# Kernel tuning notes

Measured on AMD Instinct MI355X. Metric: run time of the kernel, lower is better.

The kernel has to match this reference:

```python
import jax, jax.numpy as jnp
import numpy as np
from jax import lax

B, T, D = 4, 2048, 1024
H, DK, DV = 8, 128, 256
K_CONV = 4
EPS_RMS = 1e-5


def _causal_conv_silu(x, w, b):
    # x: (B,T,C), w: (C,1,K) depthwise, b: (C,)
    C = x.shape[-1]
    xc = jnp.transpose(x, (0, 2, 1))  # (B,C,T)
    y = lax.conv_general_dilated(
        xc, w, window_strides=(1,), padding=[(K_CONV - 1, 0)],
        dimension_numbers=('NCH', 'OIH', 'NCH'), feature_group_count=C)
    y = y + b[None, :, None]
    y = jnp.transpose(y, (0, 2, 1))  # (B,T,C)
    return jax.nn.silu(y)


def _l2norm(x, eps=1e-12):
    n = jnp.sqrt(jnp.sum(x * x, axis=-1, keepdims=True))
    return x / jnp.maximum(n, eps)


def setup_inputs() -> dict:
    key = jax.random.key(0)
    ks = jax.random.split(key, 20)
    s = 0.02
    inp = {
        'hidden_states': jax.random.normal(ks[0], (B, T, D), jnp.float32),
        'previous_state': jax.random.normal(ks[1], (B, H, DK, DV), jnp.float32) * 0.1,
        'Wq': jax.random.normal(ks[2], (D, H * DK), jnp.float32) * s,
        'Wk': jax.random.normal(ks[3], (D, H * DK), jnp.float32) * s,
        'Wv': jax.random.normal(ks[4], (D, H * DV), jnp.float32) * s,
        'Wa': jax.random.normal(ks[5], (D, H), jnp.float32) * s,
        'Wb': jax.random.normal(ks[6], (D, H), jnp.float32) * s,
        'Wg': jax.random.normal(ks[7], (D, H * DV), jnp.float32) * s,
        'Wo': jax.random.normal(ks[8], (H * DV, D), jnp.float32) * s,
        'qc_w': jax.random.normal(ks[9], (H * DK, 1, K_CONV), jnp.float32) * 0.25,
        'qc_b': jnp.zeros((H * DK,), jnp.float32),
        'kc_w': jax.random.normal(ks[10], (H * DK, 1, K_CONV), jnp.float32) * 0.25,
        'kc_b': jnp.zeros((H * DK,), jnp.float32),
        'vc_w': jax.random.normal(ks[11], (H * DV, 1, K_CONV), jnp.float32) * 0.25,
        'vc_b': jnp.zeros((H * DV,), jnp.float32),
        'o_norm_w': jnp.ones((DV,), jnp.float32),
    }
    A = jax.random.uniform(ks[12], (H,), jnp.float32, 1e-4, 16.0)
    inp['A_log'] = jnp.log(A)
    # depth_init=True: dt in [1e-4, 1e-3]
    u = jax.random.uniform(ks[13], (H,), jnp.float32)
    dt = jnp.exp(u * (np.log(1e-3) - np.log(1e-4)) + np.log(1e-4))
    inp['dt_bias'] = dt + jnp.log(-jnp.expm1(-dt))
    return inp


def reference(hidden_states, previous_state, Wq, Wk, Wv, Wa, Wb, Wg, Wo,
              qc_w, qc_b, kc_w, kc_b, vc_w, vc_b, o_norm_w, A_log, dt_bias):
    b, t, _ = hidden_states.shape
    # projections + causal depthwise conv + silu
    q = _causal_conv_silu(hidden_states @ Wq, qc_w, qc_b).reshape(b, t, H, DK)
    k = _causal_conv_silu(hidden_states @ Wk, kc_w, kc_b).reshape(b, t, H, DK)
    v = _causal_conv_silu(hidden_states @ Wv, vc_w, vc_b).reshape(b, t, H, DV)
    # gates
    g = -jnp.exp(A_log) * jax.nn.softplus(hidden_states @ Wa + dt_bias)  # (B,T,H)
    alpha = jnp.exp(g)
    beta = jax.nn.sigmoid(hidden_states @ Wb)  # (B,T,H)
    # qk L2 norm
    q = _l2norm(q)
    k = _l2norm(k)

    def step(state, xs):
        q_t, k_t, v_t, a_t, b_t = xs
        o_t = jnp.einsum('bhkv,bhk->bhv', state, q_t)  # read state BEFORE update
        delta = v_t - jnp.einsum('bhkv,bhk->bhv', state, k_t)
        state = a_t[..., None, None] * state + \
            b_t[..., None, None] * jnp.einsum('bhv,bhk->bhkv', delta, k_t)
        return state, o_t

    xs = (jnp.transpose(q, (1, 0, 2, 3)), jnp.transpose(k, (1, 0, 2, 3)),
          jnp.transpose(v, (1, 0, 2, 3)), jnp.transpose(alpha, (1, 0, 2)),
          jnp.transpose(beta, (1, 0, 2)))
    final_state, o = lax.scan(step, previous_state, xs)
    o = jnp.transpose(o, (1, 0, 2, 3))  # (B,T,H,DV)
    # gated RMSNorm per head-v dim
    gate = (hidden_states @ Wg).reshape(b, t, H, DV)
    of = o.astype(jnp.float32)
    var = jnp.mean(of * of, axis=-1, keepdims=True)
    o = (o_norm_w * (of * lax.rsqrt(var + EPS_RMS)).astype(o.dtype)) * jax.nn.sigmoid(gate)
    out = o.reshape(b, t, H * DV) @ Wo  # (B,T,D)
    return out, final_state
```

## Files before the change

kernel.cpp:

```cpp
#include <hip/hip_runtime.h>
#include <stdint.h>

typedef unsigned short u16;
typedef unsigned int u32;

#define DEVFN __device__ __forceinline__

constexpr int CB = 4;
constexpr int CT = 2048;
constexpr int CD = 1024;
constexpr int CH = 8;
constexpr int CDK = 128;
constexpr int CDV = 256;
constexpr long NROW = (long)CB * CT;

DEVFN float b2f(u16 s){ return __uint_as_float(((u32)s) << 16); }
DEVFN u16 f2b(float f){
  u32 u = __float_as_uint(f);
  u32 r = (u + 0x7fffu + ((u >> 16) & 1u)) >> 16;
  return (u16)r;
}
DEVFN float sigm(float x){ return 1.f / (1.f + expf(-x)); }
DEVFN int swz3(int r){ return (r ^ (r >> 2)) & 3; }

__global__ void cast_f32_bf16_k(const float* __restrict__ in, u16* __restrict__ out, long n4){
  long i = (long)blockIdx.x * blockDim.x + threadIdx.x;
  long stride = (long)gridDim.x * blockDim.x;
  for (; i < n4; i += stride){
    float4 v = ((const float4*)in)[i];
    ushort4 r;
    r.x = f2b(v.x); r.y = f2b(v.y); r.z = f2b(v.z); r.w = f2b(v.w);
    ((ushort4*)out)[i] = r;
  }
}

__global__ __launch_bounds__(256) void transpose_all_k(
    const float* __restrict__ Wq, const float* __restrict__ Wk, const float* __restrict__ Wv,
    const float* __restrict__ Wg, const float* __restrict__ Wo,
    u16* __restrict__ Wqkvt, u16* __restrict__ Wgt, u16* __restrict__ Wot)
{
  int bid = blockIdx.x;
  const float* W; u16* Wt; int K, N, local;
  if (bid < 1024){ W = Wq; Wt = Wqkvt; K = 1024; N = 1024; local = bid; }
  else if (bid < 2048){ W = Wk; Wt = Wqkvt + (size_t)1024 * 1024; K = 1024; N = 1024; local = bid - 1024; }
  else if (bid < 4096){ W = Wv; Wt = Wqkvt + (size_t)2048 * 1024; K = 1024; N = 2048; local = bid - 2048; }
  else if (bid < 6144){ W = Wg; Wt = Wgt; K = 1024; N = 2048; local = bid - 4096; }
  else { W = Wo; Wt = Wot; K = 2048; N = 1024; local = bid - 6144; }
  int sh = (N == 1024) ? 5 : 6;
  int bx = local & ((1 << sh) - 1), by = local >> sh;
  int n0 = bx * 32, k0 = by * 32;

  __shared__ float tile[32][33];
  int tx = threadIdx.x & 31, ty = threadIdx.x >> 5;
  #pragma unroll
  for (int i = 0; i < 4; i++)
    tile[ty + 8*i][tx] = W[(long)(k0 + ty + 8*i) * N + n0 + tx];
  __syncthreads();
  #pragma unroll
  for (int i = 0; i < 4; i++){
    int nn = ty + 8*i;
    Wt[(long)(n0 + nn) * K + k0 + tx] = f2b(tile[tx][nn]);
  }
}

typedef __bf16 bf16x8 __attribute__((ext_vector_type(8)));
typedef float f32x4 __attribute__((ext_vector_type(4)));

DEVFN void store_c(float* p, float v){ *p = v; }
DEVFN void store_c(u16* p, float v){ *p = f2b(v); }

DEVFN void gload16(const void* g, void* l){
  __builtin_amdgcn_global_load_lds((__attribute__((address_space(1))) void*)g,
                                   (__attribute__((address_space(3))) void*)l, 16, 0, 0);
}

template <typename OutT>
__global__ __launch_bounds__(256) void gemm128_k(
    const u16* __restrict__ A, const u16* __restrict__ Bt, OutT* __restrict__ C,
    int M, int N, int K)
{
  __shared__ u16 As[2][128 * 64];
  __shared__ u16 Bs[2][128 * 64];
  int tid = threadIdx.x;
  int lane = tid & 63, wv = tid >> 6;
  int wm = wv & 1, wn = wv >> 1;
  int l15 = lane & 15, lhi = lane >> 4;
  int m0 = blockIdx.y * 128, n0 = blockIdx.x * 128;
  const u16* Ab = A + (long)m0 * K;
  const u16* Bb = Bt + (long)n0 * K;

  auto stage = [&](int t, int bf){
    int k0 = t * 64;
    #pragma unroll
    for (int p = 0; p < 4; p++){
      int X = p * 256 + tid;
      int r = X >> 3, jj = X & 7;
      gload16(Ab + (long)r * K + k0 + ((jj ^ (r & 7)) * 8), &As[bf][(size_t)X * 8]);
    }
    #pragma unroll
    for (int p = 0; p < 4; p++){
      int X = p * 256 + tid;
      int r = X >> 3, jj = X & 7;
      gload16(Bb + (long)r * K + k0 + ((jj ^ (r & 7)) * 8), &Bs[bf][(size_t)X * 8]);
    }
  };

  f32x4 acc[4][4] = {};

  stage(0, 0);
  int T = K >> 6;
  for (int t = 0; t < T; t++){
    int bf = t & 1;
    if (t + 1 < T){
      stage(t + 1, bf ^ 1);
      asm volatile("s_waitcnt vmcnt(8)" ::: "memory");
    } else {
      asm volatile("s_waitcnt vmcnt(0)" ::: "memory");
    }
    __builtin_amdgcn_s_barrier();

    #pragma unroll
    for (int kk = 0; kk < 64; kk += 32){
      int s = (kk >> 3) + lhi;
      bf16x8 av[4], bv[4];
      #pragma unroll
      for (int m = 0; m < 4; m++){
        int r = wm * 64 + m * 16 + l15;
        av[m] = *(const bf16x8*)&As[bf][r * 64 + ((s ^ (r & 7)) * 8)];
      }
      #pragma unroll
      for (int n = 0; n < 4; n++){
        int r = wn * 64 + n * 16 + l15;
        bv[n] = *(const bf16x8*)&Bs[bf][r * 64 + ((s ^ (r & 7)) * 8)];
      }
      #pragma unroll
      for (int m = 0; m < 4; m++)
        #pragma unroll
        for (int n = 0; n < 4; n++)
          acc[m][n] = __builtin_amdgcn_mfma_f32_16x16x32_bf16(av[m], bv[n], acc[m][n], 0, 0, 0);
    }
    asm volatile("" ::: "memory");
    __builtin_amdgcn_s_barrier();
  }

  #pragma unroll
  for (int m = 0; m < 4; m++)
    #pragma unroll
    for (int n = 0; n < 4; n++)
      #pragma unroll
      for (int j = 0; j < 4; j++){
        long row = m0 + wm * 64 + m * 16 + lhi * 4 + j;
        long col = n0 + wn * 64 + n * 16 + l15;
        store_c(&C[row * (long)N + col], acc[m][n][j]);
      }
}

__global__ __launch_bounds__(256) void build_wab_k(
    const float* __restrict__ Wa, const float* __restrict__ Wb, u16* __restrict__ Wab)
{
  int idx = blockIdx.x * 256 + threadIdx.x;
  int c = idx >> 10, k = idx & 1023;
  float v = (c < 8) ? Wa[k * 8 + c] : Wb[k * 8 + (c - 8)];
  Wab[c * 1024 + k] = f2b(v);
}

__global__ __launch_bounds__(256) void ab_mfma_k(
    const u16* __restrict__ Xb, const u16* __restrict__ Wab,
    const float* __restrict__ A_log, const float* __restrict__ dt_bias,
    float* __restrict__ alpha, float* __restrict__ beta)
{
  __shared__ u16 Ws[16 * 1024];
  int tid = threadIdx.x, lane = tid & 63, wv = tid >> 6;
  #pragma unroll
  for (int p = 0; p < 8; p++){
    int X = p * 256 + tid;
    int r = X >> 7, s = X & 127;
    gload16(Wab + r * 1024 + (s ^ (r & 7)) * 8, &Ws[(size_t)X * 8]);
  }
  int l15 = lane & 15, lhi = lane >> 4;
  int row0 = blockIdx.x * 64 + wv * 16;
  const u16* Arow = Xb + (long)(row0 + l15) * 1024 + lhi * 8;
  __syncthreads();

  f32x4 acc = {0.f, 0.f, 0.f, 0.f};
  #pragma unroll 8
  for (int ks = 0; ks < 32; ks++){
    bf16x8 av = *(const bf16x8*)(Arow + ks * 32);
    int slot = ks * 4 + lhi;
    bf16x8 bv = *(const bf16x8*)&Ws[l15 * 1024 + (slot ^ (l15 & 7)) * 8];
    acc = __builtin_amdgcn_mfma_f32_16x16x32_bf16(av, bv, acc, 0, 0, 0);
  }

  int col = l15;
  float nA = 0.f, db = 0.f;
  if (col < 8){ nA = -expf(A_log[col]); db = dt_bias[col]; }
  #pragma unroll
  for (int j = 0; j < 4; j++){
    long row = row0 + lhi * 4 + j;
    float v = acc[j];
    if (col < 8){
      float xv = v + db;
      float sp = fmaxf(xv, 0.f) + log1pf(expf(-fabsf(xv)));
      alpha[row * 8 + col] = expf(nA * sp);
    } else {
      beta[row * 8 + (col - 8)] = sigm(v);
    }
  }
}

template<int DH, bool NORM>
__global__ __launch_bounds__(DH/2) void conv_silu8_k(
    const u16* __restrict__ pre, int cstride, const float* __restrict__ cw,
    const float* __restrict__ cb, u16* __restrict__ out)
{
  int idx = blockIdx.x;
  int h = idx & 7;
  int tg = (idx >> 3) & 255;
  int b = idx >> 11;
  int t0 = tg * 8;
  int tidx = threadIdx.x;
  int c2 = tidx * 2;
  int ch = h * DH + c2;
  const u16* base = pre + ((long)b * CT) * cstride + ch;
  float w0a = cw[ch * 4 + 0], w0b = cw[ch * 4 + 1], w0c = cw[ch * 4 + 2], w0d = cw[ch * 4 + 3];
  float w1a = cw[(ch + 1) * 4 + 0], w1b = cw[(ch + 1) * 4 + 1], w1c = cw[(ch + 1) * 4 + 2], w1d = cw[(ch + 1) * 4 + 3];
  float bs0 = cb[ch], bs1 = cb[ch + 1];

  u32 rr[11];
  #pragma unroll
  for (int i = 0; i < 11; i++){
    int t = t0 - 3 + i;
    rr[i] = (t >= 0) ? *(const u32*)(base + (long)t * cstride) : 0u;
  }
  #pragma unroll
  for (int tt = 0; tt < 8; tt++){
    int t = t0 + tt;
    float x0a = b2f((u16)(rr[tt] & 0xffffu)),     x1a = b2f((u16)(rr[tt] >> 16));
    float x0b = b2f((u16)(rr[tt + 1] & 0xffffu)), x1b = b2f((u16)(rr[tt + 1] >> 16));
    float x0c = b2f((u16)(rr[tt + 2] & 0xffffu)), x1c = b2f((u16)(rr[tt + 2] >> 16));
    float x0d = b2f((u16)(rr[tt + 3] & 0xffffu)), x1d = b2f((u16)(rr[tt + 3] >> 16));
    float a0 = fmaf(w0a, x0a, fmaf(w0b, x0b, fmaf(w0c, x0c, fmaf(w0d, x0d, bs0))));
    float a1 = fmaf(w1a, x1a, fmaf(w1b, x1b, fmaf(w1c, x1c, fmaf(w1d, x1d, bs1))));
    float y0 = a0 * sigm(a0), y1 = a1 * sigm(a1);
    if (NORM){
      float ss = y0 * y0 + y1 * y1;
      #pragma unroll
      for (int off = 1; off < 64; off <<= 1) ss += __shfl_xor(ss, off);
      float inv = 1.f / fmaxf(sqrtf(ss), 1e-12f);
      y0 *= inv; y1 *= inv;
    }
    u32 r = (u32)f2b(y0) | ((u32)f2b(y1) << 16);
    *(u32*)(out + (((long)b * CT + t) * 8 + h) * DH + c2) = r;
  }
}

__global__ __launch_bounds__(256) void chunk_meta_k(
    const u16* __restrict__ qn, const u16* __restrict__ kn, const u16* __restrict__ vn,
    const float* __restrict__ alpha, const float* __restrict__ beta,
    u16* __restrict__ TGK_g, u16* __restrict__ TVT_g, u16* __restrict__ P_g,
    u16* __restrict__ KTS_g, float* __restrict__ scal_g)
{
  int bid = blockIdx.x;
  int c = bid & 63, bh = bid >> 6;
  int b = bh >> 3, h = bh & 7;
  long rowb = (long)b * CT + c * 32;
  int tid = threadIdx.x, lane = tid & 63, wv = tid >> 6;
  int l15 = lane & 15, lhi = lane >> 4;
  int mt = wv & 1, nt = wv >> 1;

  __shared__ u16 Kc[4096], Qc[4096], Vl[8192];
  __shared__ u16 Vt[10240];
  __shared__ u16 KTG[5120];
  __shared__ u16 TinvL[1280];
  __shared__ float Al[32 * 33];
  __shared__ float al_s[32], be_s[32], cums[33], bscal[32], gsl[32];

  #pragma unroll
  for (int p = 0; p < 2; p++){
    int X = p * 256 + tid; int r = X >> 4, jj = X & 15;
    gload16(kn + ((rowb + r) * 8 + h) * 128 + (jj ^ (r & 7)) * 8, &Kc[(size_t)X * 8]);
  }
  #pragma unroll
  for (int p = 0; p < 2; p++){
    int X = p * 256 + tid; int r = X >> 4, jj = X & 15;
    gload16(qn + ((rowb + r) * 8 + h) * 128 + (jj ^ (r & 7)) * 8, &Qc[(size_t)X * 8]);
  }
  #pragma unroll
  for (int p = 0; p < 4; p++){
    int X = p * 256 + tid; int r = X >> 5, cc = X & 31;
    gload16(vn + ((rowb + r) * 8 + h) * 256 + cc * 8, &Vl[(size_t)X * 8]);
  }
  if (tid < 32) al_s[tid] = alpha[(rowb + tid) * 8 + h];
  else if (tid < 64) be_s[tid - 32] = beta[(rowb + tid - 32) * 8 + h];
  __syncthreads();
  if (tid == 0){
    float cacc = 0.f; cums[0] = 0.f;
    for (int j = 0; j < 32; j++){ cacc += logf(al_s[j]); cums[j + 1] = cacc; }
  }
  __syncthreads();
  if (tid < 32){
    bscal[tid] = be_s[tid] * expf(cums[32] - cums[tid + 1]);
    gsl[tid] = expf(cums[tid]);
  }
  asm volatile("s_waitcnt vmcnt(0)" ::: "memory");
  __syncthreads();

  #pragma unroll
  for (int i = 0; i < 16; i++){
    u32 lo = Vl[(2 * i) * 256 + tid];
    u32 hi = Vl[(2 * i + 1) * 256 + tid];
    *(u32*)&Vt[tid * 40 + 2 * i] = lo | (hi << 16);
  }

  f32x4 rk = {0.f,0.f,0.f,0.f}, rq = {0.f,0.f,0.f,0.f};
  int ra = mt * 16 + l15, rb = nt * 16 + l15;
  #pragma unroll
  for (int ks = 0; ks < 4; ks++){
    int slot = ks * 4 + lhi;
    bf16x8 ak = *(const bf16x8*)&Kc[ra * 128 + (slot ^ (ra & 7)) * 8];
    bf16x8 aq = *(const bf16x8*)&Qc[ra * 128 + (slot ^ (ra & 7)) * 8];
    bf16x8 bk = *(const bf16x8*)&Kc[rb * 128 + (slot ^ (rb & 7)) * 8];
    rk = __builtin_amdgcn_mfma_f32_16x16x32_bf16(ak, bk, rk, 0, 0, 0);
    rq = __builtin_amdgcn_mfma_f32_16x16x32_bf16(aq, bk, rq, 0, 0, 0);
  }
  int s_ = nt * 16 + l15;
  long pb_ = (long)bid * 1024;
  #pragma unroll
  for (int j = 0; j < 4; j++){
    int i_ = mt * 16 + lhi * 4 + j;
    float e = (s_ < i_) ? expf(cums[i_] - cums[s_ + 1]) * be_s[s_] : 0.f;
    Al[i_ * 33 + s_] = rk[j] * e;
    P_g[pb_ + i_ * 32 + s_] = f2b(rq[j] * e);
  }
  __syncthreads();

  if (tid < 32){
    float x[32];
    #pragma unroll
    for (int i = 0; i < 32; i++) x[i] = (i == tid) ? 1.f : 0.f;
    #pragma unroll
    for (int s = 0; s < 31; s++){
      float xs = x[s];
      #pragma unroll
      for (int i = s + 1; i < 32; i++) x[i] = fmaf(-Al[i * 33 + s], xs, x[i]);
    }
    #pragma unroll
    for (int i = 0; i < 32; i++) TinvL[i * 40 + tid] = f2b(x[i]);
    scal_g[(long)bid * 48 + tid] = gsl[tid];
    if (tid == 0) scal_g[(long)bid * 48 + 32] = expf(cums[32]);
  } else if (tid >= 64){
    int t0 = tid - 64;
    #pragma unroll
    for (int e2 = 0; e2 < 22; e2++){
      int e = t0 + e2 * 192;
      if (e < 4096){
        int k = e >> 5, s2 = e & 31;
        int slot = k >> 3;
        float kv = b2f(Kc[s2 * 128 + (slot ^ (s2 & 7)) * 8 + (k & 7)]);
        KTS_g[(long)bid * 4096 + k * 32 + s2] = f2b(kv * bscal[s2]);
        KTG[k * 40 + s2] = f2b(kv * gsl[s2]);
      }
    }
  }
  __syncthreads();

  long tb = (long)bid * 4096;
  #pragma unroll
  for (int p = 0; p < 4; p++){
    int idx = wv * 4 + p; int ts = idx >> 3, tk = idx & 7;
    bf16x8 aT = *(const bf16x8*)&TinvL[(ts * 16 + l15) * 40 + lhi * 8];
    bf16x8 bK2 = *(const bf16x8*)&KTG[(tk * 16 + l15) * 40 + lhi * 8];
    f32x4 z = {0.f,0.f,0.f,0.f};
    f32x4 d = __builtin_amdgcn_mfma_f32_16x16x32_bf16(aT, bK2, z, 0, 0, 0);
    #pragma unroll
    for (int j = 0; j < 4; j++)
      TGK_g[tb + (ts * 16 + lhi * 4 + j) * 128 + tk * 16 + l15] = f2b(d[j]);
  }
  long vb = (long)bid * 8192;
  #pragma unroll
  for (int p = 0; p < 8; p++){
    int idx = wv * 8 + p; int tv = idx >> 1, ts2 = idx & 1;
    bf16x8 aV = *(const bf16x8*)&Vt[(tv * 16 + l15) * 40 + lhi * 8];
    bf16x8 bT2 = *(const bf16x8*)&TinvL[(ts2 * 16 + l15) * 40 + lhi * 8];
    f32x4 z = {0.f,0.f,0.f,0.f};
    f32x4 d = __builtin_amdgcn_mfma_f32_16x16x32_bf16(aV, bT2, z, 0, 0, 0);
    #pragma unroll
    for (int j = 0; j < 4; j++)
      TVT_g[vb + (tv * 16 + lhi * 4 + j) * 32 + ts2 * 16 + l15] = f2b(d[j]);
  }
}

__global__ __launch_bounds__(256) void chunk_scan_k(
    const u16* __restrict__ qn, const u16* __restrict__ TGK_g, const u16* __restrict__ TVT_g,
    const u16* __restrict__ P_g, const u16* __restrict__ KTS_g,
    const float* __restrict__ scal_g, const float* __restrict__ prev,
    u16* __restrict__ obuf, float* __restrict__ fstate)
{
  int bid = blockIdx.x;
  int bh = bid & 31, vs = bid >> 5;
  int b = bh >> 3, h = bh & 7;
  int tid = threadIdx.x, lane = tid & 63, wv = tid >> 6;
  int l15 = lane & 15, lhi = lane >> 4;
  int mv = wv & 1, nn = wv >> 1;

  __shared__ u16 TG[2][4096];
  __shared__ u16 Qc[2][4096];
  __shared__ u16 TVs[2][1024];
  __shared__ float scal[2][48];
  __shared__ u16 KT[2][4096];
  __shared__ u16 Ps[2][1024];
  __shared__ u16 Sb[32 * 136];
  __shared__ u16 Ub[32 * 40];

  auto issue_g1 = [&](int c, int bf){
    long cb_ = (long)bh * 64 + c;
    const u16* Tb_ = TGK_g + cb_ * 4096;
    #pragma unroll
    for (int p = 0; p < 2; p++){
      int X = p * 256 + tid; int r = X >> 4, jj = X & 15;
      gload16(Tb_ + r * 128 + (jj ^ (r & 7)) * 8, &TG[bf][(size_t)X * 8]);
    }
    long rowb = (long)b * CT + c * 32;
    #pragma unroll
    for (int p = 0; p < 2; p++){
      int X = p * 256 + tid; int r = X >> 4, jj = X & 15;
      gload16(qn + ((rowb + r) * 8 + h) * 128 + (jj ^ (r & 7)) * 8, &Qc[bf][(size_t)X * 8]);
    }
    if (lane < 32){
      int X = wv * 32 + lane; int r = X >> 2, jj = X & 3;
      gload16(TVT_g + cb_ * 8192 + (vs * 32 + r) * 32 + (jj ^ swz3(r)) * 8, &TVs[bf][(size_t)X * 8]);
    }
    long sbase = cb_ * 48;
    #pragma unroll
    for (int p = 0; p < 3; p++){
      int X = wv * 3 + p;
      if (lane == 0) gload16(scal_g + sbase + X * 4, &scal[bf][X * 4]);
    }
  };
  auto issue_g2 = [&](int c, int bf){
    long cb_ = (long)bh * 64 + c;
    const u16* Kb_ = KTS_g + cb_ * 4096;
    #pragma unroll
    for (int p = 0; p < 2; p++){
      int X = p * 256 + tid; int r = X >> 2, jj = X & 3;
      gload16(Kb_ + (r * 4 + (jj ^ swz3(r))) * 8, &KT[bf][(size_t)X * 8]);
    }
    if (lane < 32){
      int X = wv * 32 + lane; int r = X >> 2, jj = X & 3;
      gload16(P_g + cb_ * 1024 + (r * 4 + (jj ^ swz3(r))) * 8, &Ps[bf][(size_t)X * 8]);
    }
  };

  issue_g1(0, 0);
  issue_g2(0, 0);
  f32x4 st[4];
  {
    const float* pbv = prev + ((long)bh * 128) * 256 + vs * 32;
    #pragma unroll
    for (int tt = 0; tt < 4; tt++){
      int k = (nn * 4 + tt) * 16 + l15;
      #pragma unroll
      for (int j = 0; j < 4; j++){
        int v = mv * 16 + lhi * 4 + j;
        st[tt][j] = pbv[(long)k * 256 + v];
      }
    }
  }
  #pragma unroll
  for (int tt = 0; tt < 4; tt++){
    int k = (nn * 4 + tt) * 16 + l15;
    #pragma unroll
    for (int j = 0; j < 4; j++){
      int v = mv * 16 + lhi * 4 + j;
      Sb[v * 136 + k] = f2b(st[tt][j]);
    }
  }
  asm volatile("s_waitcnt vmcnt(3) lgkmcnt(0)" ::: "memory");
  __builtin_amdgcn_s_barrier();

  int rv = mv * 16 + l15, ri = nn * 16 + l15;
  for (int c = 0; c < 64; ++c){
    int bf = c & 1;
    f32x4 us = {0.f,0.f,0.f,0.f}, o1 = {0.f,0.f,0.f,0.f};
    #pragma unroll
    for (int ks = 0; ks < 4; ks++){
      bf16x8 aS = *(const bf16x8*)&Sb[rv * 136 + ks * 32 + lhi * 8];
      int slot = ks * 4 + lhi;
      bf16x8 bT = *(const bf16x8*)&TG[bf][ri * 128 + (slot ^ (ri & 7)) * 8];
      bf16x8 bQ = *(const bf16x8*)&Qc[bf][ri * 128 + (slot ^ (ri & 7)) * 8];
      us = __builtin_amdgcn_mfma_f32_16x16x32_bf16(aS, bT, us, 0, 0, 0);
      o1 = __builtin_amdgcn_mfma_f32_16x16x32_bf16(aS, bQ, o1, 0, 0, 0);
    }
    if (c + 1 < 64) issue_g1(c + 1, bf ^ 1);
    #pragma unroll
    for (int j = 0; j < 4; j++){
      int v = mv * 16 + lhi * 4 + j;
      float tv = b2f(TVs[bf][v * 32 + ((ri >> 3) ^ swz3(v)) * 8 + (ri & 7)]);
      Ub[v * 40 + ri] = f2b(tv - us[j]);
    }
    asm volatile("s_waitcnt lgkmcnt(0)" ::: "memory");
    if (c + 1 < 64) asm volatile("s_waitcnt vmcnt(8)" ::: "memory");
    else            asm volatile("s_waitcnt vmcnt(0)" ::: "memory");
    __builtin_amdgcn_s_barrier();

    float Gt = scal[bf][32];
    f32x4 oacc;
    {
      bf16x8 aU = *(const bf16x8*)&Ub[rv * 40 + lhi * 8];
      bf16x8 bP = *(const bf16x8*)&Ps[bf][ri * 32 + (lhi ^ swz3(ri)) * 8];
      f32x4 z = {0.f,0.f,0.f,0.f};
      oacc = __builtin_amdgcn_mfma_f32_16x16x32_bf16(aU, bP, z, 0, 0, 0);
      #pragma unroll
      for (int tt = 0; tt < 4; tt++){
        int rk_ = (nn * 4 + tt) * 16 + l15;
        bf16x8 bK = *(const bf16x8*)&KT[bf][rk_ * 32 + (lhi ^ swz3(rk_)) * 8];
        f32x4 ci = st[tt] * Gt;
        st[tt] = __builtin_amdgcn_mfma_f32_16x16x32_bf16(aU, bK, ci, 0, 0, 0);
      }
    }
    {
      float gi = scal[bf][ri];
      ushort4 pk;
      pk.x = f2b(oacc[0] + gi * o1[0]);
      pk.y = f2b(oacc[1] + gi * o1[1]);
      pk.z = f2b(oacc[2] + gi * o1[2]);
      pk.w = f2b(oacc[3] + gi * o1[3]);
      *(ushort4*)&obuf[(((long)bh * CT) + c * 32 + ri) * 256 + vs * 32 + mv * 16 + lhi * 4] = pk;
    }
    if (c + 1 < 64) issue_g2(c + 1, bf ^ 1);
    #pragma unroll
    for (int tt = 0; tt < 4; tt++){
      int k = (nn * 4 + tt) * 16 + l15;
      #pragma unroll
      for (int j = 0; j < 4; j++){
        int v = mv * 16 + lhi * 4 + j;
        Sb[v * 136 + k] = f2b(st[tt][j]);
      }
    }
    asm volatile("s_waitcnt lgkmcnt(0)" ::: "memory");
    if (c + 1 < 64) asm volatile("s_waitcnt vmcnt(3)" ::: "memory");
    else            asm volatile("s_waitcnt vmcnt(0)" ::: "memory");
    __builtin_amdgcn_s_barrier();
  }

  {
    float* fb = fstate + ((long)bh * 128) * 256 + vs * 32;
    #pragma unroll
    for (int tt = 0; tt < 4; tt++){
      int k = (nn * 4 + tt) * 16 + l15;
      #pragma unroll
      for (int j = 0; j < 4; j++){
        int v = mv * 16 + lhi * 4 + j;
        fb[(long)k * 256 + v] = st[tt][j];
      }
    }
  }
}

__global__ __launch_bounds__(256) void rms_gate_k(
    const u16* __restrict__ o, const u16* __restrict__ gate,
    const float* __restrict__ nw, u16* __restrict__ ofin)
{
  long idx = (long)blockIdx.x * 4 + (threadIdx.x >> 6);
  int lane = threadIdx.x & 63;
  int h = (int)(idx & 7);
  long bt = idx >> 3;
  int b = (int)(bt >> 11);
  long t = bt & (CT - 1);
  long obase = (((long)(b * 8 + h)) * CT + t) * CDV + lane * 4;
  long base = idx * CDV + lane * 4;
  ushort4 o4 = *(const ushort4*)(o + obase);
  float ox = b2f(o4.x), oy = b2f(o4.y), oz = b2f(o4.z), ow = b2f(o4.w);
  float ss = ox*ox + oy*oy + oz*oz + ow*ow;
  #pragma unroll
  for (int off = 1; off < 64; off <<= 1) ss += __shfl_xor(ss, off);
  float r = rsqrtf(ss * (1.f / CDV) + 1e-5f);
  ushort4 g4 = *(const ushort4*)(gate + base);
  float w0 = nw[lane*4], w1 = nw[lane*4+1], w2 = nw[lane*4+2], w3 = nw[lane*4+3];
  ushort4 res;
  res.x = f2b(ox * r * w0 * sigm(b2f(g4.x)));
  res.y = f2b(oy * r * w1 * sigm(b2f(g4.y)));
  res.z = f2b(oz * r * w2 * sigm(b2f(g4.z)));
  res.w = f2b(ow * r * w3 * sigm(b2f(g4.w)));
  *(ushort4*)(ofin + base) = res;
}

extern "C" void kernel_launch(void* const* d_in, const int* in_sizes, int n_in,
                              void* d_out, int out_size, void* d_ws, size_t ws_size,
                              hipStream_t stream)
{
  (void)in_sizes; (void)n_in; (void)out_size; (void)ws_size;
  const float* X    = (const float*)d_in[0];
  const float* prev = (const float*)d_in[1];
  const float* Wq   = (const float*)d_in[2];
  const float* Wk   = (const float*)d_in[3];
  const float* Wv   = (const float*)d_in[4];
  const float* Wa   = (const float*)d_in[5];
  const float* Wb   = (const float*)d_in[6];
  const float* Wg   = (const float*)d_in[7];
  const float* Wo   = (const float*)d_in[8];
  const float* qcw  = (const float*)d_in[9];
  const float* qcb  = (const float*)d_in[10];
  const float* kcw  = (const float*)d_in[11];
  const float* kcb  = (const float*)d_in[12];
  const float* vcw  = (const float*)d_in[13];
  const float* vcb  = (const float*)d_in[14];
  const float* onw  = (const float*)d_in[15];
  const float* Alog = (const float*)d_in[16];
  const float* dtb  = (const float*)d_in[17];

  float* out = (float*)d_out;
  float* fstate = out + (long)CB * CT * CD;

  char* ws = (char*)d_ws;
  size_t off = 0;
  auto alloc = [&](size_t bytes) -> char* {
    char* p = ws + off;
    off += (bytes + 255) & ~(size_t)255;
    return p;
  };
  u16* Xb     = (u16*)alloc(NROW * CD * 2);
  u16* Wqkvt  = (u16*)alloc((size_t)4096 * 1024 * 2);
  u16* Wgt    = (u16*)alloc((size_t)2048 * 1024 * 2);
  u16* Wot    = (u16*)alloc((size_t)1024 * 2048 * 2);
  u16* qkvpre = (u16*)alloc(NROW * 4096 * 2);
  u16* gpre   = (u16*)alloc(NROW * 2048 * 2);
  float* alpha = (float*)alloc(NROW * 8 * 4);
  float* beta  = (float*)alloc(NROW * 8 * 4);
  u16* qn   = (u16*)alloc(NROW * 1024 * 2);
  u16* kn   = (u16*)alloc(NROW * 1024 * 2);
  u16* vn   = (u16*)alloc(NROW * 2048 * 2);
  u16* ofin = (u16*)alloc(NROW * 2048 * 2);
  u16* Wab  = (u16*)alloc((size_t)16 * 1024 * 2);
  u16* TGK_g  = Xb;
  u16* TVT_g  = ofin;
  u16* obuf   = qkvpre;
  u16* P_g    = qkvpre + (size_t)16777216;
  float* scal_g = (float*)(qkvpre + (size_t)18874368);
  u16* KTS_g  = qkvpre + (size_t)19136512;

  cast_f32_bf16_k<<<2048, 256, 0, stream>>>(X, Xb, NROW * CD / 4);
  build_wab_k<<<64, 256, 0, stream>>>(Wa, Wb, Wab);
  transpose_all_k<<<8192, 256, 0, stream>>>(Wq, Wk, Wv, Wg, Wo, Wqkvt, Wgt, Wot);

  gemm128_k<u16><<<dim3(32, 64), 256, 0, stream>>>(Xb, Wqkvt, qkvpre, 8192, 4096, 1024);
  gemm128_k<u16><<<dim3(16, 64), 256, 0, stream>>>(Xb, Wgt, gpre, 8192, 2048, 1024);
  ab_mfma_k<<<128, 256, 0, stream>>>(Xb, Wab, Alog, dtb, alpha, beta);

  conv_silu8_k<128, true><<<CB * (CT / 8) * CH, 64, 0, stream>>>(qkvpre, 4096, qcw, qcb, qn);
  conv_silu8_k<128, true><<<CB * (CT / 8) * CH, 64, 0, stream>>>(qkvpre + 1024, 4096, kcw, kcb, kn);
  conv_silu8_k<256, false><<<CB * (CT / 8) * CH, 128, 0, stream>>>(qkvpre + 2048, 4096, vcw, vcb, vn);

  chunk_meta_k<<<2048, 256, 0, stream>>>(qn, kn, vn, alpha, beta,
                                         TGK_g, TVT_g, P_g, KTS_g, scal_g);
  chunk_scan_k<<<256, 256, 0, stream>>>(qn, TGK_g, TVT_g, P_g, KTS_g, scal_g,
                                        prev, obuf, fstate);

  rms_gate_k<<<CB * CT * CH / 4, 256, 0, stream>>>(obuf, gpre, onw, ofin);
  gemm128_k<float><<<dim3(8, 64), 256, 0, stream>>>(ofin, Wot, out, 8192, 1024, 2048);
}
```

Before: 387.5 us.

## Split chunk scan across more blocks, swizzle GEMM tile order, raise MFMA priority

The chunk scan kernel now gives each block a 16-wide slice of the value dimension with 2 waves instead of a 32-wide slice with 4 waves. This doubles the grid to 512 blocks so more CUs work on the sequential recurrence. Global-to-LDS loads and wait counts are adjusted to match, and s_setprio brackets the MFMA sections. The GEMM kernel also remaps block indices with a stride-8 swizzle to change tile traversal order for cache locality. The cost is that each scan block re-fetches the full TG/Q/KT tiles, so total global traffic per chunk roughly doubles.

```diff
diff --git a/kernel.cpp b/kernel.cpp
--- a/kernel.cpp
+++ b/kernel.cpp
@@ -85,7 +85,12 @@
   int lane = tid & 63, wv = tid >> 6;
   int wm = wv & 1, wn = wv >> 1;
   int l15 = lane & 15, lhi = lane >> 4;
-  int m0 = blockIdx.y * 128, n0 = blockIdx.x * 128;
+  u32 gx = gridDim.x;
+  u32 nwg = gx * gridDim.y;
+  u32 lin = blockIdx.y * gx + blockIdx.x;
+  u32 sw = (lin & 7) * (nwg >> 3) + (lin >> 3);
+  int bx = (int)(sw % gx), by = (int)(sw / gx);
+  int m0 = by * 128, n0 = bx * 128;
   const u16* Ab = A + (long)m0 * K;
   const u16* Bb = Bt + (long)n0 * K;
 
@@ -390,7 +395,7 @@
   }
 }
 
-__global__ __launch_bounds__(256) void chunk_scan_k(
+__global__ __launch_bounds__(128) void chunk_scan_k(
     const u16* __restrict__ qn, const u16* __restrict__ TGK_g, const u16* __restrict__ TVT_g,
     const u16* __restrict__ P_g, const u16* __restrict__ KTS_g,
     const float* __restrict__ scal_g, const float* __restrict__ prev,
@@ -399,54 +404,50 @@
   int bid = blockIdx.x;
   int bh = bid & 31, vs = bid >> 5;
   int b = bh >> 3, h = bh & 7;
-  int tid = threadIdx.x, lane = tid & 63, wv = tid >> 6;
+  int tid = threadIdx.x, lane = tid & 63, nn = tid >> 6;
   int l15 = lane & 15, lhi = lane >> 4;
-  int mv = wv & 1, nn = wv >> 1;
 
   __shared__ u16 TG[2][4096];
   __shared__ u16 Qc[2][4096];
-  __shared__ u16 TVs[2][1024];
+  __shared__ u16 TVs[2][512];
   __shared__ float scal[2][48];
   __shared__ u16 KT[2][4096];
   __shared__ u16 Ps[2][1024];
-  __shared__ u16 Sb[32 * 136];
-  __shared__ u16 Ub[32 * 40];
+  __shared__ u16 Sb[16 * 136];
+  __shared__ u16 Ub[16 * 40];
 
   auto issue_g1 = [&](int c, int bf){
     long cb_ = (long)bh * 64 + c;
     const u16* Tb_ = TGK_g + cb_ * 4096;
     #pragma unroll
-    for (int p = 0; p < 2; p++){
-      int X = p * 256 + tid; int r = X >> 4, jj = X & 15;
+    for (int p = 0; p < 4; p++){
+      int X = p * 128 + tid; int r = X >> 4, jj = X & 15;
       gload16(Tb_ + r * 128 + (jj ^ (r & 7)) * 8, &TG[bf][(size_t)X * 8]);
     }
     long rowb = (long)b * CT + c * 32;
     #pragma unroll
-    for (int p = 0; p < 2; p++){
-      int X = p * 256 + tid; int r = X >> 4, jj = X & 15;
+    for (int p = 0; p < 4; p++){
+      int X = p * 128 + tid; int r = X >> 4, jj = X & 15;
       gload16(qn + ((rowb + r) * 8 + h) * 128 + (jj ^ (r & 7)) * 8, &Qc[bf][(size_t)X * 8]);
     }
-    if (lane < 32){
-      int X = wv * 32 + lane; int r = X >> 2, jj = X & 3;
-      gload16(TVT_g + cb_ * 8192 + (vs * 32 + r) * 32 + (jj ^ swz3(r)) * 8, &TVs[bf][(size_t)X * 8]);
-    }
-    long sbase = cb_ * 48;
-    #pragma unroll
-    for (int p = 0; p < 3; p++){
-      int X = wv * 3 + p;
-      if (lane == 0) gload16(scal_g + sbase + X * 4, &scal[bf][X * 4]);
-    }
+    {
+      int X = lane;
+      int r = X >> 2, jj = X & 3;
+      gload16(TVT_g + cb_ * 8192 + (vs * 16 + r) * 32 + (jj ^ swz3(r)) * 8, &TVs[bf][(size_t)X * 8]);
+    }
+    if (lane < 12)
+      gload16(scal_g + cb_ * 48 + lane * 4, (char*)&scal[bf][0] + lane * 16);
   };
   auto issue_g2 = [&](int c, int bf){
     long cb_ = (long)bh * 64 + c;
     const u16* Kb_ = KTS_g + cb_ * 4096;
     #pragma unroll
-    for (int p = 0; p < 2; p++){
-      int X = p * 256 + tid; int r = X >> 2, jj = X & 3;
+    for (int p = 0; p < 4; p++){
+      int X = p * 128 + tid; int r = X >> 2, jj = X & 3;
       gload16(Kb_ + (r * 4 + (jj ^ swz3(r))) * 8, &KT[bf][(size_t)X * 8]);
     }
-    if (lane < 32){
-      int X = wv * 32 + lane; int r = X >> 2, jj = X & 3;
+    {
+      int X = tid; int r = X >> 2, jj = X & 3;
       gload16(P_g + cb_ * 1024 + (r * 4 + (jj ^ swz3(r))) * 8, &Ps[bf][(size_t)X * 8]);
     }
   };
@@ -455,13 +456,13 @@
   issue_g2(0, 0);
   f32x4 st[4];
   {
-    const float* pbv = prev + ((long)bh * 128) * 256 + vs * 32;
+    const float* pbv = prev + ((long)bh * 128) * 256 + vs * 16;
     #pragma unroll
     for (int tt = 0; tt < 4; tt++){
       int k = (nn * 4 + tt) * 16 + l15;
       #pragma unroll
       for (int j = 0; j < 4; j++){
-        int v = mv * 16 + lhi * 4 + j;
+        int v = lhi * 4 + j;
         st[tt][j] = pbv[(long)k * 256 + v];
       }
     }
@@ -471,17 +472,18 @@
     int k = (nn * 4 + tt) * 16 + l15;
     #pragma unroll
     for (int j = 0; j < 4; j++){
-      int v = mv * 16 + lhi * 4 + j;
+      int v = lhi * 4 + j;
       Sb[v * 136 + k] = f2b(st[tt][j]);
     }
   }
-  asm volatile("s_waitcnt vmcnt(3) lgkmcnt(0)" ::: "memory");
+  asm volatile("s_waitcnt vmcnt(5) lgkmcnt(0)" ::: "memory");
   __builtin_amdgcn_s_barrier();
 
-  int rv = mv * 16 + l15, ri = nn * 16 + l15;
+  int rv = l15, ri = nn * 16 + l15;
   for (int c = 0; c < 64; ++c){
     int bf = c & 1;
     f32x4 us = {0.f,0.f,0.f,0.f}, o1 = {0.f,0.f,0.f,0.f};
+    __builtin_amdgcn_s_setprio(1);
     #pragma unroll
     for (int ks = 0; ks < 4; ks++){
       bf16x8 aS = *(const bf16x8*)&Sb[rv * 136 + ks * 32 + lhi * 8];
@@ -491,15 +493,16 @@
       us = __builtin_amdgcn_mfma_f32_16x16x32_bf16(aS, bT, us, 0, 0, 0);
       o1 = __builtin_amdgcn_mfma_f32_16x16x32_bf16(aS, bQ, o1, 0, 0, 0);
     }
+    __builtin_amdgcn_s_setprio(0);
     if (c + 1 < 64) issue_g1(c + 1, bf ^ 1);
     #pragma unroll
     for (int j = 0; j < 4; j++){
-      int v = mv * 16 + lhi * 4 + j;
+      int v = lhi * 4 + j;
       float tv = b2f(TVs[bf][v * 32 + ((ri >> 3) ^ swz3(v)) * 8 + (ri & 7)]);
       Ub[v * 40 + ri] = f2b(tv - us[j]);
     }
     asm volatile("s_waitcnt lgkmcnt(0)" ::: "memory");
-    if (c + 1 < 64) asm volatile("s_waitcnt vmcnt(8)" ::: "memory");
+    if (c + 1 < 64) asm volatile("s_waitcnt vmcnt(10)" ::: "memory");
     else            asm volatile("s_waitcnt vmcnt(0)" ::: "memory");
     __builtin_amdgcn_s_barrier();
 
@@ -509,6 +512,7 @@
       bf16x8 aU = *(const bf16x8*)&Ub[rv * 40 + lhi * 8];
       bf16x8 bP = *(const bf16x8*)&Ps[bf][ri * 32 + (lhi ^ swz3(ri)) * 8];
       f32x4 z = {0.f,0.f,0.f,0.f};
+      __builtin_amdgcn_s_setprio(1);
       oacc = __builtin_amdgcn_mfma_f32_16x16x32_bf16(aU, bP, z, 0, 0, 0);
       #pragma unroll
       for (int tt = 0; tt < 4; tt++){
@@ -517,6 +521,7 @@
         f32x4 ci = st[tt] * Gt;
         st[tt] = __builtin_amdgcn_mfma_f32_16x16x32_bf16(aU, bK, ci, 0, 0, 0);
       }
+      __builtin_amdgcn_s_setprio(0);
     }
     {
       float gi = scal[bf][ri];
@@ -525,7 +530,7 @@
       pk.y = f2b(oacc[1] + gi * o1[1]);
       pk.z = f2b(oacc[2] + gi * o1[2]);
       pk.w = f2b(oacc[3] + gi * o1[3]);
-      *(ushort4*)&obuf[(((long)bh * CT) + c * 32 + ri) * 256 + vs * 32 + mv * 16 + lhi * 4] = pk;
+      *(ushort4*)&obuf[(((long)bh * CT) + c * 32 + ri) * 256 + vs * 16 + lhi * 4] = pk;
     }
     if (c + 1 < 64) issue_g2(c + 1, bf ^ 1);
     #pragma unroll
@@ -533,24 +538,24 @@
       int k = (nn * 4 + tt) * 16 + l15;
       #pragma unroll
       for (int j = 0; j < 4; j++){
-        int v = mv * 16 + lhi * 4 + j;
+        int v = lhi * 4 + j;
         Sb[v * 136 + k] = f2b(st[tt][j]);
       }
     }
     asm volatile("s_waitcnt lgkmcnt(0)" ::: "memory");
-    if (c + 1 < 64) asm volatile("s_waitcnt vmcnt(3)" ::: "memory");
+    if (c + 1 < 64) asm volatile("s_waitcnt vmcnt(5)" ::: "memory");
     else            asm volatile("s_waitcnt vmcnt(0)" ::: "memory");
     __builtin_amdgcn_s_barrier();
   }
 
   {
-    float* fb = fstate + ((long)bh * 128) * 256 + vs * 32;
+    float* fb = fstate + ((long)bh * 128) * 256 + vs * 16;
     #pragma unroll
     for (int tt = 0; tt < 4; tt++){
       int k = (nn * 4 + tt) * 16 + l15;
       #pragma unroll
       for (int j = 0; j < 4; j++){
-        int v = mv * 16 + lhi * 4 + j;
+        int v = lhi * 4 + j;
         fb[(long)k * 256 + v] = st[tt][j];
       }
     }
@@ -653,7 +658,7 @@
 
   chunk_meta_k<<<2048, 256, 0, stream>>>(qn, kn, vn, alpha, beta,
                                          TGK_g, TVT_g, P_g, KTS_g, scal_g);
-  chunk_scan_k<<<256, 256, 0, stream>>>(qn, TGK_g, TVT_g, P_g, KTS_g, scal_g,
+  chunk_scan_k<<<512, 128, 0, stream>>>(qn, TGK_g, TVT_g, P_g, KTS_g, scal_g,
                                         prev, obuf, fstate);
 
   rms_gate_k<<<CB * CT * CH / 4, 256, 0, stream>>>(obuf, gpre, onw, ofin);
```

Result: slower. 414.7 us (+7.0%).
